# Optimization experiments

Measured on AMD Instinct MI355X. Metric: run time of the kernel, lower is better.

## Reference

```python
import jax, jax.numpy as jnp
import numpy as np

B, S, D, H = 4, 2048, 1024, 16
HD = D // H

def setup_inputs() -> dict:
    key = jax.random.key(0)
    k1, k2, k3, k4, k5 = jax.random.split(key, 5)
    sc = 1.0 / np.sqrt(D)
    return {
        "x": jax.random.normal(k1, (B, S, D), dtype=jnp.float32),
        "w_qkv": jax.random.normal(k2, (D, 3 * D), dtype=jnp.float32) * sc,
        "b_qkv": jnp.zeros((3 * D,), dtype=jnp.float32),
        "w_proj": jax.random.normal(k3, (D, D), dtype=jnp.float32) * sc,
        "b_proj": jnp.zeros((D,), dtype=jnp.float32),
    }

def reference(x, w_qkv, b_qkv, w_proj, b_proj):
    bsz, seq_len, dim = x.shape
    qkv = x @ w_qkv + b_qkv                      # [B,S,3D]
    q, k, v = jnp.split(qkv, 3, axis=2)
    q = q.reshape(bsz, seq_len, H, HD).transpose(0, 2, 1, 3)  # [B,H,S,hd]
    k = k.reshape(bsz, seq_len, H, HD).transpose(0, 2, 1, 3)
    v = v.reshape(bsz, seq_len, H, HD).transpose(0, 2, 1, 3)
    att = jnp.einsum('bhqd,bhkd->bhqk', q, k) * (1.0 / np.sqrt(HD))
    causal = jnp.tril(jnp.ones((seq_len, seq_len), dtype=bool))
    att = jnp.where(causal[None, None], att, -jnp.inf)
    att = jax.nn.softmax(att, axis=-1)
    y = jnp.einsum('bhqk,bhkd->bhqd', att, v)
    y = y.transpose(0, 2, 1, 3).reshape(bsz, seq_len, dim)
    return y @ w_proj + b_proj
```

## Files before the change

### kernel.cpp

```cpp
#include <hip/hip_runtime.h>
#include <cstdint>
#include <cstddef>

typedef float  f32x4  __attribute__((ext_vector_type(4)));
typedef __bf16 bf16x8 __attribute__((ext_vector_type(8)));
typedef __bf16 bf16x4 __attribute__((ext_vector_type(4)));

#define DEVI static __device__ __forceinline__

DEVI f32x4 mfma_bf16(bf16x8 a, bf16x8 b, f32x4 c) {
  return __builtin_amdgcn_mfma_f32_16x16x32_bf16(a, b, c, 0, 0, 0);
}

DEVI void gload_lds16(const void* g, void* l) {
  __builtin_amdgcn_global_load_lds(
      (const __attribute__((address_space(1))) void*)g,
      (__attribute__((address_space(3))) void*)l, 16, 0, 0);
}

__global__ __launch_bounds__(256) void k_prep(
    const float* __restrict__ x, __bf16* __restrict__ xb,
    const float* __restrict__ w_qkv, __bf16* __restrict__ wqkvT,
    const float* __restrict__ w_proj, __bf16* __restrict__ wprojT) {
  __shared__ __bf16 tile[64][65];
  const int idx = blockIdx.x;
  if (idx < 8192) {
    int i = idx * 256 + threadIdx.x;
    float4 v = reinterpret_cast<const float4*>(x)[i];
    bf16x4 r;
    r.x = (__bf16)v.x; r.y = (__bf16)v.y; r.z = (__bf16)v.z; r.w = (__bf16)v.w;
    reinterpret_cast<bf16x4*>(xb)[i] = r;
    return;
  }
  const float* src; __bf16* dst; int R, C, bx, by;
  if (idx < 8960) {
    int id2 = idx - 8192; bx = id2 % 48; by = id2 / 48;
    src = w_qkv; dst = wqkvT; R = 1024; C = 3072;
  } else {
    int id2 = idx - 8960; bx = id2 % 16; by = id2 / 16;
    src = w_proj; dst = wprojT; R = 1024; C = 1024;
  }
  const int tx = threadIdx.x & 63, ty = threadIdx.x >> 6;
  const int r0 = by * 64, c0 = bx * 64;
#pragma unroll
  for (int i = 0; i < 16; ++i) {
    int r = ty * 16 + i;
    tile[r][tx] = (__bf16)src[(size_t)(r0 + r) * C + c0 + tx];
  }
  __syncthreads();
#pragma unroll
  for (int i = 0; i < 16; ++i) {
    int c = ty * 16 + i;
    dst[(size_t)(c0 + c) * R + r0 + tx] = tile[tx][c];
  }
}

template <int MODE>
__global__ __launch_bounds__(256, 2) void k_gemm_bt(
    const __bf16* __restrict__ A, const __bf16* __restrict__ Bt,
    const float* __restrict__ bias, void* __restrict__ Cv,
    __bf16* __restrict__ VT,
    int M, int N, int K, int nbx) {
  __shared__ __bf16 As[128 * 64];
  __shared__ __bf16 Bs[128 * 64];
  const int t = threadIdx.x;
  const int w = t >> 6, lane = t & 63;
  const int l15 = lane & 15, lg = lane >> 4;
  const int m0 = (blockIdx.x / nbx) * 128;
  const int n0 = (blockIdx.x % nbx) * 128;
  const int wr = w >> 1, wc = w & 1;
  const int lrow = lane >> 3, lslot = lane & 7;

  f32x4 acc[4][4] = {};

  const int nK = K >> 6;
  for (int kt = 0; kt < nK; ++kt) {
    const __bf16* Ab = A + (size_t)m0 * K + kt * 64;
    const __bf16* Bb = Bt + (size_t)n0 * K + kt * 64;
#pragma unroll
    for (int c = 0; c < 4; ++c) {
      int seg = w * 4 + c;
      int row = seg * 8 + lrow;
      int cb = (lslot ^ (row & 7)) << 4;
      gload_lds16((const char*)(Ab + (size_t)row * K) + cb, (char*)As + seg * 1024);
      gload_lds16((const char*)(Bb + (size_t)row * K) + cb, (char*)Bs + seg * 1024);
    }
    __syncthreads();
#pragma unroll
    for (int ks = 0; ks < 2; ++ks) {
      bf16x8 af[4], bfr[4];
      const int cb = ks * 64 + (lg << 4);
#pragma unroll
      for (int m = 0; m < 4; ++m) {
        int row = wr * 64 + m * 16 + l15;
        af[m] = *(const bf16x8*)((const char*)As + row * 128 + (cb ^ ((row & 7) << 4)));
      }
#pragma unroll
      for (int n = 0; n < 4; ++n) {
        int row = wc * 64 + n * 16 + l15;
        bfr[n] = *(const bf16x8*)((const char*)Bs + row * 128 + (cb ^ ((row & 7) << 4)));
      }
#pragma unroll
      for (int m = 0; m < 4; ++m)
#pragma unroll
        for (int n = 0; n < 4; ++n)
          acc[m][n] = mfma_bf16(af[m], bfr[n], acc[m][n]);
    }
    __syncthreads();
  }

  const bool vsec = (MODE == 0) && (VT != nullptr) && (n0 >= 2048);
#pragma unroll
  for (int n = 0; n < 4; ++n) {
    const int gcol = n0 + wc * 64 + n * 16 + l15;
    const float bv = bias ? bias[gcol] : 0.0f;
#pragma unroll
    for (int m = 0; m < 4; ++m) {
      const int grow = m0 + wr * 64 + m * 16 + (lg << 2);
      if (vsec) {
        const int hd = gcol - 2048;
        const int b = grow >> 11, s0v = grow & 2047;
        const int nib = (s0v >> 2) & 15;
        const int nib2 = (nib < 4) ? 2 * nib : (nib < 8) ? 2 * nib - 7
                        : (nib < 12) ? 2 * nib - 8 : 2 * nib - 15;
        const int sp = (s0v & ~63) | (nib2 << 2);
        bf16x4 pkv;
#pragma unroll
        for (int r = 0; r < 4; ++r) pkv[r] = (__bf16)(acc[m][n][r] + bv);
        *(bf16x4*)(VT + ((size_t)(b * 16) * 64 + hd) * 2048 + sp) = pkv;
      } else {
#pragma unroll
        for (int r = 0; r < 4; ++r) {
          float v = acc[m][n][r] + bv;
          if (MODE == 0)
            ((__bf16*)Cv)[(size_t)(grow + r) * N + gcol] = (__bf16)v;
          else
            ((float*)Cv)[(size_t)(grow + r) * N + gcol] = v;
        }
      }
    }
  }
}

__global__ __launch_bounds__(512, 2) void k_attn(
    const __bf16* __restrict__ qkv,
    const __bf16* __restrict__ VT,
    __bf16* __restrict__ Y) {
  __shared__ __bf16 kbuf[2][64 * 64];
  __shared__ __bf16 vbuf[2][64 * 64];
  const int t = threadIdx.x, w = t >> 6, lane = t & 63;
  const int l15 = lane & 15, lg = lane >> 4;
  const int bid = blockIdx.x;
  const int g = bid >> 6;
  const int qt = (g < 4) ? 15 - g : (g < 8) ? g - 4 : (g < 12) ? 19 - g : g - 8;
  const int bh = bid & 63;
  const int b = bh >> 4, h = bh & 15;
  const int q0 = qt * 128;
  const int nkv = 2 * qt + 2;
  const float SCL = 0.125f * 1.44269504f;

  const size_t qrow = (size_t)(b * 2048 + q0 + w * 16 + l15);
  const bf16x8 qf0 = *(const bf16x8*)(qkv + qrow * 3072 + h * 64 + lg * 8);
  const bf16x8 qf1 = *(const bf16x8*)(qkv + qrow * 3072 + h * 64 + 32 + lg * 8);

  const __bf16* kg = qkv + (size_t)(b * 2048) * 3072 + 1024 + h * 64;
  const __bf16* vg = VT + (size_t)bh * 64 * 2048;

  const int srow = t >> 3, sslot = t & 7;
  const int sb = (sslot ^ (srow & 7)) << 4;
  auto stage = [&](int bi, int kvi) {
    gload_lds16((const char*)(kg + (size_t)(kvi * 64 + srow) * 3072) + sb,
                (char*)kbuf[bi] + w * 1024);
    gload_lds16((const char*)(vg + (size_t)srow * 2048 + kvi * 64) + sb,
                (char*)vbuf[bi] + w * 1024);
  };

  f32x4 o[4] = {};
  float mr = -1e30f, lr = 0.0f;

  stage(0, 0);
  asm volatile("s_waitcnt vmcnt(0)" ::: "memory");
  __syncthreads();

  for (int kv = 0; kv < nkv; ++kv) {
    if (kv + 1 < nkv) stage((kv + 1) & 1, kv + 1);
    const char* kb = (const char*)kbuf[kv & 1];
    const char* vb = (const char*)vbuf[kv & 1];

    f32x4 s[4] = {};
    __builtin_amdgcn_s_setprio(1);
#pragma unroll
    for (int nb = 0; nb < 4; ++nb) {
      int row = nb * 16 + l15;
      int sw = (row & 7) << 4;
      bf16x8 k0 = *(const bf16x8*)(kb + row * 128 + ((lg * 16) ^ sw));
      bf16x8 k1 = *(const bf16x8*)(kb + row * 128 + ((64 + lg * 16) ^ sw));
      s[nb] = mfma_bf16(k0, qf0, s[nb]);
      s[nb] = mfma_bf16(k1, qf1, s[nb]);
    }
    __builtin_amdgcn_s_setprio(0);

    if (((kv + 1) << 6) > q0 + w * 16) {
      const int qg = q0 + w * 16 + l15;
#pragma unroll
      for (int nb = 0; nb < 4; ++nb)
#pragma unroll
        for (int r = 0; r < 4; ++r)
          if (kv * 64 + nb * 16 + lg * 4 + r > qg) s[nb][r] = -1e30f;
    }

    float a0 = fmaxf(fmaxf(s[0][0], s[0][1]), s[0][2]);
    float a1 = fmaxf(fmaxf(s[0][3], s[1][0]), s[1][1]);
    float a2 = fmaxf(fmaxf(s[1][2], s[1][3]), s[2][0]);
    float a3 = fmaxf(fmaxf(s[2][1], s[2][2]), s[2][3]);
    float a4 = fmaxf(fmaxf(s[3][0], s[3][1]), s[3][2]);
    float pm = fmaxf(fmaxf(fmaxf(a0, a1), a2), fmaxf(fmaxf(a3, a4), s[3][3]));
    pm = fmaxf(pm, __shfl_xor(pm, 16));
    pm = fmaxf(pm, __shfl_xor(pm, 32));
    pm *= SCL;

    if (!__all(pm <= mr + 8.0f)) {
      float nm = fmaxf(mr, pm);
      float alpha = __builtin_amdgcn_exp2f(mr - nm);
      lr *= alpha;
      mr = nm;
#pragma unroll
      for (int r = 0; r < 4; ++r) {
        float aO = __shfl(alpha, lg * 4 + r);
        o[0][r] *= aO; o[1][r] *= aO; o[2][r] *= aO; o[3][r] *= aO;
      }
    }

    float ps = 0.0f;
    bf16x4 pk[4];
#pragma unroll
    for (int nb = 0; nb < 4; ++nb) {
      f32x4 pe;
#pragma unroll
      for (int r = 0; r < 4; ++r)
        pe[r] = __builtin_amdgcn_exp2f(fmaf(s[nb][r], SCL, -mr));
      ps += (pe[0] + pe[1]) + (pe[2] + pe[3]);
      pk[nb][0] = (__bf16)pe[0]; pk[nb][1] = (__bf16)pe[1];
      pk[nb][2] = (__bf16)pe[2]; pk[nb][3] = (__bf16)pe[3];
    }
    ps += __shfl_xor(ps, 16);
    ps += __shfl_xor(ps, 32);
    lr += ps;

    const bf16x8 pf0 = __builtin_shufflevector(pk[0], pk[1], 0, 1, 2, 3, 4, 5, 6, 7);
    const bf16x8 pf1 = __builtin_shufflevector(pk[2], pk[3], 0, 1, 2, 3, 4, 5, 6, 7);
    __builtin_amdgcn_s_setprio(1);
#pragma unroll
    for (int nb = 0; nb < 4; ++nb) {
      int row = nb * 16 + l15;
      int sw = (row & 7) << 4;
      bf16x8 v0 = *(const bf16x8*)(vb + row * 128 + ((lg * 16) ^ sw));
      bf16x8 v1 = *(const bf16x8*)(vb + row * 128 + ((64 + lg * 16) ^ sw));
      o[nb] = mfma_bf16(pf0, v0, o[nb]);
      o[nb] = mfma_bf16(pf1, v1, o[nb]);
    }
    __builtin_amdgcn_s_setprio(0);
    asm volatile("s_waitcnt vmcnt(0)" ::: "memory");
    __syncthreads();
  }

  float lO[4];
#pragma unroll
  for (int r = 0; r < 4; ++r) lO[r] = __shfl(lr, lg * 4 + r);
#pragma unroll
  for (int nb = 0; nb < 4; ++nb)
#pragma unroll
    for (int r = 0; r < 4; ++r) {
      float v = o[nb][r] / lO[r];
      size_t row = (size_t)(b * 2048 + q0 + w * 16 + lg * 4 + r);
      Y[row * 1024 + h * 64 + nb * 16 + l15] = (__bf16)v;
    }
}

extern "C" void kernel_launch(void* const* d_in, const int* in_sizes, int n_in,
                              void* d_out, int out_size, void* d_ws, size_t ws_size,
                              hipStream_t stream) {
  const float* x      = (const float*)d_in[0];
  const float* w_qkv  = (const float*)d_in[1];
  const float* b_qkv  = (const float*)d_in[2];
  const float* w_proj = (const float*)d_in[3];
  const float* b_proj = (const float*)d_in[4];
  float* out = (float*)d_out;

  char* ws = (char*)d_ws;
  const size_t MB = 1024 * 1024;
  __bf16* xb     = (__bf16*)(ws);
  __bf16* wqkvT  = (__bf16*)(ws + 16 * MB);
  __bf16* wprojT = (__bf16*)(ws + 22 * MB);
  __bf16* qkv    = (__bf16*)(ws + 24 * MB);
  __bf16* VT     = (__bf16*)(ws + 72 * MB);
  __bf16* Y      = (__bf16*)(ws + 88 * MB);

  k_prep<<<dim3(9216), 256, 0, stream>>>(x, xb, w_qkv, wqkvT, w_proj, wprojT);
  k_gemm_bt<0><<<dim3(64 * 24), 256, 0, stream>>>(xb, wqkvT, b_qkv, qkv, VT, 8192, 3072, 1024, 24);
  k_attn<<<dim3(1024), 512, 0, stream>>>(qkv, VT, Y);
  k_gemm_bt<1><<<dim3(64 * 8), 256, 0, stream>>>(Y, wprojT, b_proj, out, nullptr, 8192, 1024, 1024, 8);
}
```

Baseline: 165.4 us.

## Pair complementary 64-row causal query tiles per 4-wave attention block

The attention kernel now uses 256-thread blocks, each handling two 64-row query tiles (p and 31-p) one after the other, instead of one 128-row tile with 8 waves. This gives every block the same total KV work (33 tiles), so causal load imbalance across blocks goes away. K/V staging is split into two loads per thread to fill the same 64x64 LDS tiles with half the threads. The cost is half as many waves per block sharing each staged K/V tile, so each tile is reused less, and the two passes run serially inside a block.

```diff
diff --git a/kernel.cpp b/kernel.cpp
--- a/kernel.cpp
+++ b/kernel.cpp
@@ -142,7 +142,7 @@
   }
 }
 
-__global__ __launch_bounds__(512, 2) void k_attn(
+__global__ __launch_bounds__(256, 2) void k_attn(
     const __bf16* __restrict__ qkv,
     const __bf16* __restrict__ VT,
     __bf16* __restrict__ Y) {
@@ -151,130 +151,138 @@
   const int t = threadIdx.x, w = t >> 6, lane = t & 63;
   const int l15 = lane & 15, lg = lane >> 4;
   const int bid = blockIdx.x;
-  const int g = bid >> 6;
-  const int qt = (g < 4) ? 15 - g : (g < 8) ? g - 4 : (g < 12) ? 19 - g : g - 8;
+  const int p = bid >> 6;
   const int bh = bid & 63;
   const int b = bh >> 4, h = bh & 15;
-  const int q0 = qt * 128;
-  const int nkv = 2 * qt + 2;
   const float SCL = 0.125f * 1.44269504f;
-
-  const size_t qrow = (size_t)(b * 2048 + q0 + w * 16 + l15);
-  const bf16x8 qf0 = *(const bf16x8*)(qkv + qrow * 3072 + h * 64 + lg * 8);
-  const bf16x8 qf1 = *(const bf16x8*)(qkv + qrow * 3072 + h * 64 + 32 + lg * 8);
 
   const __bf16* kg = qkv + (size_t)(b * 2048) * 3072 + 1024 + h * 64;
   const __bf16* vg = VT + (size_t)bh * 64 * 2048;
 
-  const int srow = t >> 3, sslot = t & 7;
-  const int sb = (sslot ^ (srow & 7)) << 4;
+  const int srow = lane >> 3, sslot = lane & 7;
   auto stage = [&](int bi, int kvi) {
-    gload_lds16((const char*)(kg + (size_t)(kvi * 64 + srow) * 3072) + sb,
-                (char*)kbuf[bi] + w * 1024);
-    gload_lds16((const char*)(vg + (size_t)srow * 2048 + kvi * 64) + sb,
-                (char*)vbuf[bi] + w * 1024);
+#pragma unroll
+    for (int i = 0; i < 2; ++i) {
+      int row = i * 32 + w * 8 + srow;
+      int sb = (sslot ^ (row & 7)) << 4;
+      gload_lds16((const char*)(kg + (size_t)(kvi * 64 + row) * 3072) + sb,
+                  (char*)kbuf[bi] + i * 4096 + w * 1024);
+      gload_lds16((const char*)(vg + (size_t)row * 2048 + kvi * 64) + sb,
+                  (char*)vbuf[bi] + i * 4096 + w * 1024);
+    }
   };
 
-  f32x4 o[4] = {};
-  float mr = -1e30f, lr = 0.0f;
-
-  stage(0, 0);
-  asm volatile("s_waitcnt vmcnt(0)" ::: "memory");
-  __syncthreads();
-
-  for (int kv = 0; kv < nkv; ++kv) {
-    if (kv + 1 < nkv) stage((kv + 1) & 1, kv + 1);
-    const char* kb = (const char*)kbuf[kv & 1];
-    const char* vb = (const char*)vbuf[kv & 1];
-
-    f32x4 s[4] = {};
-    __builtin_amdgcn_s_setprio(1);
-#pragma unroll
-    for (int nb = 0; nb < 4; ++nb) {
-      int row = nb * 16 + l15;
-      int sw = (row & 7) << 4;
-      bf16x8 k0 = *(const bf16x8*)(kb + row * 128 + ((lg * 16) ^ sw));
-      bf16x8 k1 = *(const bf16x8*)(kb + row * 128 + ((64 + lg * 16) ^ sw));
-      s[nb] = mfma_bf16(k0, qf0, s[nb]);
-      s[nb] = mfma_bf16(k1, qf1, s[nb]);
-    }
-    __builtin_amdgcn_s_setprio(0);
-
-    if (((kv + 1) << 6) > q0 + w * 16) {
-      const int qg = q0 + w * 16 + l15;
-#pragma unroll
-      for (int nb = 0; nb < 4; ++nb)
-#pragma unroll
-        for (int r = 0; r < 4; ++r)
-          if (kv * 64 + nb * 16 + lg * 4 + r > qg) s[nb][r] = -1e30f;
-    }
-
-    float a0 = fmaxf(fmaxf(s[0][0], s[0][1]), s[0][2]);
-    float a1 = fmaxf(fmaxf(s[0][3], s[1][0]), s[1][1]);
-    float a2 = fmaxf(fmaxf(s[1][2], s[1][3]), s[2][0]);
-    float a3 = fmaxf(fmaxf(s[2][1], s[2][2]), s[2][3]);
-    float a4 = fmaxf(fmaxf(s[3][0], s[3][1]), s[3][2]);
-    float pm = fmaxf(fmaxf(fmaxf(a0, a1), a2), fmaxf(fmaxf(a3, a4), s[3][3]));
-    pm = fmaxf(pm, __shfl_xor(pm, 16));
-    pm = fmaxf(pm, __shfl_xor(pm, 32));
-    pm *= SCL;
-
-    if (!__all(pm <= mr + 8.0f)) {
-      float nm = fmaxf(mr, pm);
-      float alpha = __builtin_amdgcn_exp2f(mr - nm);
-      lr *= alpha;
-      mr = nm;
-#pragma unroll
-      for (int r = 0; r < 4; ++r) {
-        float aO = __shfl(alpha, lg * 4 + r);
-        o[0][r] *= aO; o[1][r] *= aO; o[2][r] *= aO; o[3][r] *= aO;
-      }
-    }
-
-    float ps = 0.0f;
-    bf16x4 pk[4];
-#pragma unroll
-    for (int nb = 0; nb < 4; ++nb) {
-      f32x4 pe;
-#pragma unroll
-      for (int r = 0; r < 4; ++r)
-        pe[r] = __builtin_amdgcn_exp2f(fmaf(s[nb][r], SCL, -mr));
-      ps += (pe[0] + pe[1]) + (pe[2] + pe[3]);
-      pk[nb][0] = (__bf16)pe[0]; pk[nb][1] = (__bf16)pe[1];
-      pk[nb][2] = (__bf16)pe[2]; pk[nb][3] = (__bf16)pe[3];
-    }
-    ps += __shfl_xor(ps, 16);
-    ps += __shfl_xor(ps, 32);
-    lr += ps;
-
-    const bf16x8 pf0 = __builtin_shufflevector(pk[0], pk[1], 0, 1, 2, 3, 4, 5, 6, 7);
-    const bf16x8 pf1 = __builtin_shufflevector(pk[2], pk[3], 0, 1, 2, 3, 4, 5, 6, 7);
-    __builtin_amdgcn_s_setprio(1);
-#pragma unroll
-    for (int nb = 0; nb < 4; ++nb) {
-      int row = nb * 16 + l15;
-      int sw = (row & 7) << 4;
-      bf16x8 v0 = *(const bf16x8*)(vb + row * 128 + ((lg * 16) ^ sw));
-      bf16x8 v1 = *(const bf16x8*)(vb + row * 128 + ((64 + lg * 16) ^ sw));
-      o[nb] = mfma_bf16(pf0, v0, o[nb]);
-      o[nb] = mfma_bf16(pf1, v1, o[nb]);
-    }
-    __builtin_amdgcn_s_setprio(0);
+#pragma unroll 1
+  for (int ps = 0; ps < 2; ++ps) {
+    const int qt = ps ? 31 - p : p;
+    const int q0 = qt << 6;
+    const int nkv = qt + 1;
+
+    const size_t qrow = (size_t)(b * 2048 + q0 + w * 16 + l15);
+    const bf16x8 qf0 = *(const bf16x8*)(qkv + qrow * 3072 + h * 64 + lg * 8);
+    const bf16x8 qf1 = *(const bf16x8*)(qkv + qrow * 3072 + h * 64 + 32 + lg * 8);
+
+    f32x4 o[4] = {};
+    float mr = -1e30f, lr = 0.0f;
+
+    stage(0, 0);
     asm volatile("s_waitcnt vmcnt(0)" ::: "memory");
     __syncthreads();
-  }
-
-  float lO[4];
-#pragma unroll
-  for (int r = 0; r < 4; ++r) lO[r] = __shfl(lr, lg * 4 + r);
-#pragma unroll
-  for (int nb = 0; nb < 4; ++nb)
-#pragma unroll
-    for (int r = 0; r < 4; ++r) {
-      float v = o[nb][r] / lO[r];
-      size_t row = (size_t)(b * 2048 + q0 + w * 16 + lg * 4 + r);
-      Y[row * 1024 + h * 64 + nb * 16 + l15] = (__bf16)v;
-    }
+
+    for (int kv = 0; kv < nkv; ++kv) {
+      if (kv + 1 < nkv) stage((kv + 1) & 1, kv + 1);
+      const char* kb = (const char*)kbuf[kv & 1];
+      const char* vb = (const char*)vbuf[kv & 1];
+
+      f32x4 s[4] = {};
+      __builtin_amdgcn_s_setprio(1);
+#pragma unroll
+      for (int nb = 0; nb < 4; ++nb) {
+        int row = nb * 16 + l15;
+        int sw = (row & 7) << 4;
+        bf16x8 k0 = *(const bf16x8*)(kb + row * 128 + ((lg * 16) ^ sw));
+        bf16x8 k1 = *(const bf16x8*)(kb + row * 128 + ((64 + lg * 16) ^ sw));
+        s[nb] = mfma_bf16(k0, qf0, s[nb]);
+        s[nb] = mfma_bf16(k1, qf1, s[nb]);
+      }
+      __builtin_amdgcn_s_setprio(0);
+
+      if (kv == qt) {
+        const int qg = q0 + w * 16 + l15;
+#pragma unroll
+        for (int nb = 0; nb < 4; ++nb)
+#pragma unroll
+          for (int r = 0; r < 4; ++r)
+            if (kv * 64 + nb * 16 + lg * 4 + r > qg) s[nb][r] = -1e30f;
+      }
+
+      float a0 = fmaxf(fmaxf(s[0][0], s[0][1]), s[0][2]);
+      float a1 = fmaxf(fmaxf(s[0][3], s[1][0]), s[1][1]);
+      float a2 = fmaxf(fmaxf(s[1][2], s[1][3]), s[2][0]);
+      float a3 = fmaxf(fmaxf(s[2][1], s[2][2]), s[2][3]);
+      float a4 = fmaxf(fmaxf(s[3][0], s[3][1]), s[3][2]);
+      float pm = fmaxf(fmaxf(fmaxf(a0, a1), a2), fmaxf(fmaxf(a3, a4), s[3][3]));
+      pm = fmaxf(pm, __shfl_xor(pm, 16));
+      pm = fmaxf(pm, __shfl_xor(pm, 32));
+      pm *= SCL;
+
+      if (!__all(pm <= mr + 8.0f)) {
+        float nm = fmaxf(mr, pm);
+        float alpha = __builtin_amdgcn_exp2f(mr - nm);
+        lr *= alpha;
+        mr = nm;
+#pragma unroll
+        for (int r = 0; r < 4; ++r) {
+          float aO = __shfl(alpha, lg * 4 + r);
+          o[0][r] *= aO; o[1][r] *= aO; o[2][r] *= aO; o[3][r] *= aO;
+        }
+      }
+
+      float psum = 0.0f;
+      bf16x4 pk[4];
+#pragma unroll
+      for (int nb = 0; nb < 4; ++nb) {
+        f32x4 pe;
+#pragma unroll
+        for (int r = 0; r < 4; ++r)
+          pe[r] = __builtin_amdgcn_exp2f(fmaf(s[nb][r], SCL, -mr));
+        psum += (pe[0] + pe[1]) + (pe[2] + pe[3]);
+        pk[nb][0] = (__bf16)pe[0]; pk[nb][1] = (__bf16)pe[1];
+        pk[nb][2] = (__bf16)pe[2]; pk[nb][3] = (__bf16)pe[3];
+      }
+      psum += __shfl_xor(psum, 16);
+      psum += __shfl_xor(psum, 32);
+      lr += psum;
+
+      const bf16x8 pf0 = __builtin_shufflevector(pk[0], pk[1], 0, 1, 2, 3, 4, 5, 6, 7);
+      const bf16x8 pf1 = __builtin_shufflevector(pk[2], pk[3], 0, 1, 2, 3, 4, 5, 6, 7);
+      __builtin_amdgcn_s_setprio(1);
+#pragma unroll
+      for (int nb = 0; nb < 4; ++nb) {
+        int row = nb * 16 + l15;
+        int sw = (row & 7) << 4;
+        bf16x8 v0 = *(const bf16x8*)(vb + row * 128 + ((lg * 16) ^ sw));
+        bf16x8 v1 = *(const bf16x8*)(vb + row * 128 + ((64 + lg * 16) ^ sw));
+        o[nb] = mfma_bf16(pf0, v0, o[nb]);
+        o[nb] = mfma_bf16(pf1, v1, o[nb]);
+      }
+      __builtin_amdgcn_s_setprio(0);
+      asm volatile("s_waitcnt vmcnt(0)" ::: "memory");
+      __syncthreads();
+    }
+
+    float lO[4];
+#pragma unroll
+    for (int r = 0; r < 4; ++r) lO[r] = __shfl(lr, lg * 4 + r);
+#pragma unroll
+    for (int nb = 0; nb < 4; ++nb)
+#pragma unroll
+      for (int r = 0; r < 4; ++r) {
+        float v = o[nb][r] / lO[r];
+        size_t row = (size_t)(b * 2048 + q0 + w * 16 + lg * 4 + r);
+        Y[row * 1024 + h * 64 + nb * 16 + l15] = (__bf16)v;
+      }
+  }
 }
 
 extern "C" void kernel_launch(void* const* d_in, const int* in_sizes, int n_in,
@@ -298,6 +306,6 @@
 
   k_prep<<<dim3(9216), 256, 0, stream>>>(x, xb, w_qkv, wqkvT, w_proj, wprojT);
   k_gemm_bt<0><<<dim3(64 * 24), 256, 0, stream>>>(xb, wqkvT, b_qkv, qkv, VT, 8192, 3072, 1024, 24);
-  k_attn<<<dim3(1024), 512, 0, stream>>>(qkv, VT, Y);
+  k_attn<<<dim3(1024), 256, 0, stream>>>(qkv, VT, Y);
   k_gemm_bt<1><<<dim3(64 * 8), 256, 0, stream>>>(Y, wprojT, b_proj, out, nullptr, 8192, 1024, 1024, 8);
 }
```

Measured after the change: 173.5 us. 5.0% more time.

## Make attention kernel persistent with atomic longest-first work queue

Applied to the files above, without the earlier changes.

The attention kernel becomes persistent: 768 blocks repeatedly claim (q-tile, batch-head) tasks from a global atomic counter, in longest-first order (largest causal q-tile first). The counter is reset inside the prep kernel. The aim is better load balance for the triangular causal workload and less tail imbalance than the previous static block-to-tile interleave. The cost is an atomic plus an extra barrier per task, and the counter is reset only in-stream, so it depends on launch ordering.

```diff
diff --git a/kernel.cpp b/kernel.cpp
--- a/kernel.cpp
+++ b/kernel.cpp
@@ -21,9 +21,11 @@
 __global__ __launch_bounds__(256) void k_prep(
     const float* __restrict__ x, __bf16* __restrict__ xb,
     const float* __restrict__ w_qkv, __bf16* __restrict__ wqkvT,
-    const float* __restrict__ w_proj, __bf16* __restrict__ wprojT) {
+    const float* __restrict__ w_proj, __bf16* __restrict__ wprojT,
+    unsigned int* __restrict__ cnt) {
   __shared__ __bf16 tile[64][65];
   const int idx = blockIdx.x;
+  if (idx == 0 && threadIdx.x == 0) *cnt = 0u;
   if (idx < 8192) {
     int i = idx * 256 + threadIdx.x;
     float4 v = reinterpret_cast<const float4*>(x)[i];
@@ -145,136 +147,144 @@
 __global__ __launch_bounds__(512, 2) void k_attn(
     const __bf16* __restrict__ qkv,
     const __bf16* __restrict__ VT,
-    __bf16* __restrict__ Y) {
+    __bf16* __restrict__ Y,
+    unsigned int* __restrict__ cnt) {
   __shared__ __bf16 kbuf[2][64 * 64];
   __shared__ __bf16 vbuf[2][64 * 64];
+  __shared__ unsigned int task_sh;
   const int t = threadIdx.x, w = t >> 6, lane = t & 63;
   const int l15 = lane & 15, lg = lane >> 4;
-  const int bid = blockIdx.x;
-  const int g = bid >> 6;
-  const int qt = (g < 4) ? 15 - g : (g < 8) ? g - 4 : (g < 12) ? 19 - g : g - 8;
-  const int bh = bid & 63;
-  const int b = bh >> 4, h = bh & 15;
-  const int q0 = qt * 128;
-  const int nkv = 2 * qt + 2;
   const float SCL = 0.125f * 1.44269504f;
-
-  const size_t qrow = (size_t)(b * 2048 + q0 + w * 16 + l15);
-  const bf16x8 qf0 = *(const bf16x8*)(qkv + qrow * 3072 + h * 64 + lg * 8);
-  const bf16x8 qf1 = *(const bf16x8*)(qkv + qrow * 3072 + h * 64 + 32 + lg * 8);
-
-  const __bf16* kg = qkv + (size_t)(b * 2048) * 3072 + 1024 + h * 64;
-  const __bf16* vg = VT + (size_t)bh * 64 * 2048;
 
   const int srow = t >> 3, sslot = t & 7;
   const int sb = (sslot ^ (srow & 7)) << 4;
-  auto stage = [&](int bi, int kvi) {
-    gload_lds16((const char*)(kg + (size_t)(kvi * 64 + srow) * 3072) + sb,
-                (char*)kbuf[bi] + w * 1024);
-    gload_lds16((const char*)(vg + (size_t)srow * 2048 + kvi * 64) + sb,
-                (char*)vbuf[bi] + w * 1024);
-  };
-
-  f32x4 o[4] = {};
-  float mr = -1e30f, lr = 0.0f;
-
-  stage(0, 0);
-  asm volatile("s_waitcnt vmcnt(0)" ::: "memory");
-  __syncthreads();
-
-  for (int kv = 0; kv < nkv; ++kv) {
-    if (kv + 1 < nkv) stage((kv + 1) & 1, kv + 1);
-    const char* kb = (const char*)kbuf[kv & 1];
-    const char* vb = (const char*)vbuf[kv & 1];
-
-    f32x4 s[4] = {};
-    __builtin_amdgcn_s_setprio(1);
-#pragma unroll
-    for (int nb = 0; nb < 4; ++nb) {
-      int row = nb * 16 + l15;
-      int sw = (row & 7) << 4;
-      bf16x8 k0 = *(const bf16x8*)(kb + row * 128 + ((lg * 16) ^ sw));
-      bf16x8 k1 = *(const bf16x8*)(kb + row * 128 + ((64 + lg * 16) ^ sw));
-      s[nb] = mfma_bf16(k0, qf0, s[nb]);
-      s[nb] = mfma_bf16(k1, qf1, s[nb]);
-    }
-    __builtin_amdgcn_s_setprio(0);
-
-    if (((kv + 1) << 6) > q0 + w * 16) {
-      const int qg = q0 + w * 16 + l15;
-#pragma unroll
-      for (int nb = 0; nb < 4; ++nb)
-#pragma unroll
-        for (int r = 0; r < 4; ++r)
-          if (kv * 64 + nb * 16 + lg * 4 + r > qg) s[nb][r] = -1e30f;
-    }
-
-    float a0 = fmaxf(fmaxf(s[0][0], s[0][1]), s[0][2]);
-    float a1 = fmaxf(fmaxf(s[0][3], s[1][0]), s[1][1]);
-    float a2 = fmaxf(fmaxf(s[1][2], s[1][3]), s[2][0]);
-    float a3 = fmaxf(fmaxf(s[2][1], s[2][2]), s[2][3]);
-    float a4 = fmaxf(fmaxf(s[3][0], s[3][1]), s[3][2]);
-    float pm = fmaxf(fmaxf(fmaxf(a0, a1), a2), fmaxf(fmaxf(a3, a4), s[3][3]));
-    pm = fmaxf(pm, __shfl_xor(pm, 16));
-    pm = fmaxf(pm, __shfl_xor(pm, 32));
-    pm *= SCL;
-
-    if (!__all(pm <= mr + 8.0f)) {
-      float nm = fmaxf(mr, pm);
-      float alpha = __builtin_amdgcn_exp2f(mr - nm);
-      lr *= alpha;
-      mr = nm;
-#pragma unroll
-      for (int r = 0; r < 4; ++r) {
-        float aO = __shfl(alpha, lg * 4 + r);
-        o[0][r] *= aO; o[1][r] *= aO; o[2][r] *= aO; o[3][r] *= aO;
-      }
-    }
-
-    float ps = 0.0f;
-    bf16x4 pk[4];
-#pragma unroll
-    for (int nb = 0; nb < 4; ++nb) {
-      f32x4 pe;
-#pragma unroll
-      for (int r = 0; r < 4; ++r)
-        pe[r] = __builtin_amdgcn_exp2f(fmaf(s[nb][r], SCL, -mr));
-      ps += (pe[0] + pe[1]) + (pe[2] + pe[3]);
-      pk[nb][0] = (__bf16)pe[0]; pk[nb][1] = (__bf16)pe[1];
-      pk[nb][2] = (__bf16)pe[2]; pk[nb][3] = (__bf16)pe[3];
-    }
-    ps += __shfl_xor(ps, 16);
-    ps += __shfl_xor(ps, 32);
-    lr += ps;
-
-    const bf16x8 pf0 = __builtin_shufflevector(pk[0], pk[1], 0, 1, 2, 3, 4, 5, 6, 7);
-    const bf16x8 pf1 = __builtin_shufflevector(pk[2], pk[3], 0, 1, 2, 3, 4, 5, 6, 7);
-    __builtin_amdgcn_s_setprio(1);
-#pragma unroll
-    for (int nb = 0; nb < 4; ++nb) {
-      int row = nb * 16 + l15;
-      int sw = (row & 7) << 4;
-      bf16x8 v0 = *(const bf16x8*)(vb + row * 128 + ((lg * 16) ^ sw));
-      bf16x8 v1 = *(const bf16x8*)(vb + row * 128 + ((64 + lg * 16) ^ sw));
-      o[nb] = mfma_bf16(pf0, v0, o[nb]);
-      o[nb] = mfma_bf16(pf1, v1, o[nb]);
-    }
-    __builtin_amdgcn_s_setprio(0);
+
+  while (true) {
+    if (t == 0) task_sh = atomicAdd(cnt, 1u);
+    __syncthreads();
+    const unsigned int task = task_sh;
+    if (task >= 1024u) break;
+    const int qt = 15 - (int)(task >> 6);
+    const int bh = (int)(task & 63u);
+    const int b = bh >> 4, h = bh & 15;
+    const int q0 = qt << 7;
+    const int nkv = 2 * qt + 2;
+
+    const __bf16* kg = qkv + (size_t)(b * 2048) * 3072 + 1024 + h * 64;
+    const __bf16* vg = VT + (size_t)bh * 64 * 2048;
+
+    const size_t qrow = (size_t)(b * 2048 + q0 + w * 16 + l15);
+    const bf16x8 qf0 = *(const bf16x8*)(qkv + qrow * 3072 + h * 64 + lg * 8);
+    const bf16x8 qf1 = *(const bf16x8*)(qkv + qrow * 3072 + h * 64 + 32 + lg * 8);
+
+    f32x4 o[4] = {};
+    float mr = -1e30f, lr = 0.0f;
+
+    gload_lds16((const char*)(kg + (size_t)srow * 3072) + sb, (char*)kbuf[0] + w * 1024);
+    gload_lds16((const char*)(vg + (size_t)srow * 2048) + sb, (char*)vbuf[0] + w * 1024);
     asm volatile("s_waitcnt vmcnt(0)" ::: "memory");
     __syncthreads();
-  }
-
-  float lO[4];
-#pragma unroll
-  for (int r = 0; r < 4; ++r) lO[r] = __shfl(lr, lg * 4 + r);
-#pragma unroll
-  for (int nb = 0; nb < 4; ++nb)
-#pragma unroll
-    for (int r = 0; r < 4; ++r) {
-      float v = o[nb][r] / lO[r];
-      size_t row = (size_t)(b * 2048 + q0 + w * 16 + lg * 4 + r);
-      Y[row * 1024 + h * 64 + nb * 16 + l15] = (__bf16)v;
+
+    for (int kv = 0; kv < nkv; ++kv) {
+      if (kv + 1 < nkv) {
+        const int kvi = kv + 1, bi = kvi & 1;
+        gload_lds16((const char*)(kg + (size_t)(kvi * 64 + srow) * 3072) + sb,
+                    (char*)kbuf[bi] + w * 1024);
+        gload_lds16((const char*)(vg + (size_t)srow * 2048 + kvi * 64) + sb,
+                    (char*)vbuf[bi] + w * 1024);
+      }
+      const char* kb = (const char*)kbuf[kv & 1];
+      const char* vb = (const char*)vbuf[kv & 1];
+
+      f32x4 s[4] = {};
+      __builtin_amdgcn_s_setprio(1);
+#pragma unroll
+      for (int nb = 0; nb < 4; ++nb) {
+        int row = nb * 16 + l15;
+        int sw = (row & 7) << 4;
+        bf16x8 k0 = *(const bf16x8*)(kb + row * 128 + ((lg * 16) ^ sw));
+        bf16x8 k1 = *(const bf16x8*)(kb + row * 128 + ((64 + lg * 16) ^ sw));
+        s[nb] = mfma_bf16(k0, qf0, s[nb]);
+        s[nb] = mfma_bf16(k1, qf1, s[nb]);
+      }
+      __builtin_amdgcn_s_setprio(0);
+
+      if (((kv + 1) << 6) > q0 + w * 16) {
+        const int qg = q0 + w * 16 + l15;
+#pragma unroll
+        for (int nb = 0; nb < 4; ++nb)
+#pragma unroll
+          for (int r = 0; r < 4; ++r)
+            if (kv * 64 + nb * 16 + lg * 4 + r > qg) s[nb][r] = -1e30f;
+      }
+
+      float a0 = fmaxf(fmaxf(s[0][0], s[0][1]), s[0][2]);
+      float a1 = fmaxf(fmaxf(s[0][3], s[1][0]), s[1][1]);
+      float a2 = fmaxf(fmaxf(s[1][2], s[1][3]), s[2][0]);
+      float a3 = fmaxf(fmaxf(s[2][1], s[2][2]), s[2][3]);
+      float a4 = fmaxf(fmaxf(s[3][0], s[3][1]), s[3][2]);
+      float pm = fmaxf(fmaxf(fmaxf(a0, a1), a2), fmaxf(fmaxf(a3, a4), s[3][3]));
+      pm = fmaxf(pm, __shfl_xor(pm, 16));
+      pm = fmaxf(pm, __shfl_xor(pm, 32));
+      pm *= SCL;
+
+      if (!__all(pm <= mr + 8.0f)) {
+        float nm = fmaxf(mr, pm);
+        float alpha = __builtin_amdgcn_exp2f(mr - nm);
+        lr *= alpha;
+        mr = nm;
+#pragma unroll
+        for (int r = 0; r < 4; ++r) {
+          float aO = __shfl(alpha, lg * 4 + r);
+          o[0][r] *= aO; o[1][r] *= aO; o[2][r] *= aO; o[3][r] *= aO;
+        }
+      }
+
+      float psum = 0.0f;
+      bf16x4 pk[4];
+#pragma unroll
+      for (int nb = 0; nb < 4; ++nb) {
+        f32x4 pe;
+#pragma unroll
+        for (int r = 0; r < 4; ++r)
+          pe[r] = __builtin_amdgcn_exp2f(fmaf(s[nb][r], SCL, -mr));
+        psum += (pe[0] + pe[1]) + (pe[2] + pe[3]);
+        pk[nb][0] = (__bf16)pe[0]; pk[nb][1] = (__bf16)pe[1];
+        pk[nb][2] = (__bf16)pe[2]; pk[nb][3] = (__bf16)pe[3];
+      }
+      psum += __shfl_xor(psum, 16);
+      psum += __shfl_xor(psum, 32);
+      lr += psum;
+
+      const bf16x8 pf0 = __builtin_shufflevector(pk[0], pk[1], 0, 1, 2, 3, 4, 5, 6, 7);
+      const bf16x8 pf1 = __builtin_shufflevector(pk[2], pk[3], 0, 1, 2, 3, 4, 5, 6, 7);
+      __builtin_amdgcn_s_setprio(1);
+#pragma unroll
+      for (int nb = 0; nb < 4; ++nb) {
+        int row = nb * 16 + l15;
+        int sw = (row & 7) << 4;
+        bf16x8 v0 = *(const bf16x8*)(vb + row * 128 + ((lg * 16) ^ sw));
+        bf16x8 v1 = *(const bf16x8*)(vb + row * 128 + ((64 + lg * 16) ^ sw));
+        o[nb] = mfma_bf16(pf0, v0, o[nb]);
+        o[nb] = mfma_bf16(pf1, v1, o[nb]);
+      }
+      __builtin_amdgcn_s_setprio(0);
+      asm volatile("s_waitcnt vmcnt(0)" ::: "memory");
+      __syncthreads();
     }
+
+    float lO[4];
+#pragma unroll
+    for (int r = 0; r < 4; ++r) lO[r] = __shfl(lr, lg * 4 + r);
+#pragma unroll
+    for (int nb = 0; nb < 4; ++nb)
+#pragma unroll
+      for (int r = 0; r < 4; ++r) {
+        float v = o[nb][r] / lO[r];
+        size_t row = (size_t)(b * 2048 + q0 + w * 16 + lg * 4 + r);
+        Y[row * 1024 + h * 64 + nb * 16 + l15] = (__bf16)v;
+      }
+  }
 }
 
 extern "C" void kernel_launch(void* const* d_in, const int* in_sizes, int n_in,
@@ -295,9 +305,10 @@
   __bf16* qkv    = (__bf16*)(ws + 24 * MB);
   __bf16* VT     = (__bf16*)(ws + 72 * MB);
   __bf16* Y      = (__bf16*)(ws + 88 * MB);
-
-  k_prep<<<dim3(9216), 256, 0, stream>>>(x, xb, w_qkv, wqkvT, w_proj, wprojT);
+  unsigned int* cnt = (unsigned int*)(ws + 104 * MB);
+
+  k_prep<<<dim3(9216), 256, 0, stream>>>(x, xb, w_qkv, wqkvT, w_proj, wprojT, cnt);
   k_gemm_bt<0><<<dim3(64 * 24), 256, 0, stream>>>(xb, wqkvT, b_qkv, qkv, VT, 8192, 3072, 1024, 24);
-  k_attn<<<dim3(1024), 512, 0, stream>>>(qkv, VT, Y);
+  k_attn<<<dim3(768), 512, 0, stream>>>(qkv, VT, Y, cnt);
   k_gemm_bt<1><<<dim3(64 * 8), 256, 0, stream>>>(Y, wprojT, b_proj, out, nullptr, 8192, 1024, 1024, 8);
 }
```

Result: slower. 178.5 us (+8.0%).
